# Kernel tuning notes

Hardware: AMD Instinct MI355X
Metric: run time of the kernel (lower is better)

The kernel has to match this reference:

```python
import math
import jax, jax.numpy as jnp
import numpy as np

S, K, Q, N, D, H = 512, 512, 64, 262144, 256, 8
DH = D // H
EPS = 1e-5


def layer_norm(x, g, b):
    mu = jnp.mean(x, axis=-1, keepdims=True)
    var = jnp.mean((x - mu) ** 2, axis=-1, keepdims=True)
    return (x - mu) / jnp.sqrt(var + EPS) * g + b


def setup_inputs() -> dict:
    key = jax.random.key(0)
    ks = jax.random.split(key, 12)
    s = 1.0 / math.sqrt(D)
    x = jax.random.normal(ks[0], (N, D), dtype=jnp.float32)
    target_ids = jax.random.randint(ks[1], (S, K), 0, N)
    # unique query slots per sample (matches torch per-slot overwrite with distinct ids)
    perm = jax.vmap(lambda k: jax.random.permutation(k, K))(jax.random.split(ks[2], S))
    add_ids = perm[:, :Q]
    return {
        "x": x,
        "target_ids": target_ids,
        "add_ids": add_ids,
        "Wq": jax.random.uniform(ks[3], (D, D), jnp.float32, -s, s),
        "bq": jnp.zeros((D,), jnp.float32),
        "Wk": jax.random.uniform(ks[4], (D, D), jnp.float32, -s, s),
        "bk": jnp.zeros((D,), jnp.float32),
        "Wv": jax.random.uniform(ks[5], (D, D), jnp.float32, -s, s),
        "bv": jnp.zeros((D,), jnp.float32),
        "g1": jnp.ones((D,), jnp.float32),
        "b1": jnp.zeros((D,), jnp.float32),
        "Wl": jax.random.uniform(ks[6], (D, D), jnp.float32, -s, s),
        "bl": jnp.zeros((D,), jnp.float32),
        "g2": jnp.ones((D,), jnp.float32),
        "b2": jnp.zeros((D,), jnp.float32),
    }


def reference(x, target_ids, add_ids, Wq, bq, Wk, bk, Wv, bv, g1, b1, Wl, bl, g2, b2):
    # gather per-sample node subsets
    key_t = x[target_ids]                                   # [S, K, D]
    query = jnp.take_along_axis(key_t, add_ids[:, :, None], axis=1)  # [S, Q, D]
    # MAB projections
    Qp = (query @ Wq.T + bq).reshape(S, Q, H, DH)
    Kp = (key_t @ Wk.T + bk).reshape(S, K, H, DH)
    Vp = (key_t @ Wv.T + bv).reshape(S, K, H, DH)
    # attention with original scaling by sqrt(dim_V) (full D, not per-head)
    scores = jnp.einsum("sqhd,skhd->shqk", Qp, Kp) / math.sqrt(D)
    A = jax.nn.softmax(scores, axis=-1)
    out = Qp + jnp.einsum("shqk,skhd->sqhd", A, Vp)          # residual on Q_
    out = out.reshape(S, Q, D)
    out = layer_norm(out, g1, b1)
    out = out + jax.nn.relu(out @ Wl.T + bl)
    out = layer_norm(out, g2, b2)                            # [S, Q, D]
    # scatter back into per-sample slots, then residual with key
    x_fuse = jnp.zeros((S, K, D), out.dtype)
    x_fuse = x_fuse.at[jnp.arange(S)[:, None], add_ids].set(out)
    x_fuse = x_fuse + key_t
    return x_fuse.reshape(S * K, D)
```

## Files before the change

kernel.cpp:

```cpp
#include <hip/hip_runtime.h>

#define S_ 512
#define K_ 512
#define Q_ 64
#define D_ 256
#define H_ 8
#define SK_ (S_*K_)
#define SQ_ (S_*Q_)

typedef float f32x4 __attribute__((ext_vector_type(4)));
typedef short bf16x8 __attribute__((ext_vector_type(8)));
typedef short bf16x4 __attribute__((ext_vector_type(4)));

__device__ __forceinline__ short f2bf(float f) {
  unsigned u = __builtin_bit_cast(unsigned, f);
  u += 0x7fffu + ((u >> 16) & 1u);
  return (short)(u >> 16);
}
__device__ __forceinline__ float bf2f(short s) {
  unsigned u = ((unsigned)(unsigned short)s) << 16;
  return __builtin_bit_cast(float, u);
}

__device__ __forceinline__ void async_copy16(short* lds, const short* g) {
  __builtin_amdgcn_global_load_lds(
      (const __attribute__((address_space(1))) void*)g,
      (__attribute__((address_space(3))) void*)lds, 16, 0, 0);
}

__global__ void cvt_w_kernel(const float* Wq, const float* Wk, const float* Wv,
                             const float* Wl, short* out) {
  int i = blockIdx.x * 256 + threadIdx.x;
  const float* src = (i < 65536) ? Wq : (i < 131072) ? Wk : (i < 196608) ? Wv : Wl;
  out[i] = f2bf(src[i & 65535]);
}

__global__ void gather_kernel(const float* x, const int* tid, short* kb) {
  int g = blockIdx.x * 256 + threadIdx.x;
  int row = g >> 5, e = (g & 31) * 8;
  int src = tid[row];
  f32x4 v0 = *(const f32x4*)(x + (size_t)src * 256 + e);
  f32x4 v1 = *(const f32x4*)(x + (size_t)src * 256 + e + 4);
  bf16x8 o;
#pragma unroll
  for (int j = 0; j < 4; j++) { o[j] = f2bf(v0[j]); o[j + 4] = f2bf(v1[j]); }
  *(bf16x8*)(kb + (size_t)row * 256 + e) = o;
}

__global__ void expand_kernel(const short* kb, float* dout) {
  int g = blockIdx.x * 256 + threadIdx.x;
  bf16x8 v = *(const bf16x8*)(kb + (size_t)g * 8);
  f32x4 a, b;
#pragma unroll
  for (int j = 0; j < 4; j++) { a[j] = bf2f(v[j]); b[j] = bf2f(v[j + 4]); }
  *(f32x4*)(dout + (size_t)g * 8) = a;
  *(f32x4*)(dout + (size_t)g * 8 + 4) = b;
}

template<int INDEXED, int CT>
__global__ __launch_bounds__(256, 2) void gemm2_kernel(const short* A, const int* aid,
                                                       const short* Wb, const float* bias,
                                                       short* Cp) {
  __shared__ short As[128 * 256];
  int w = threadIdx.x >> 6, lane = threadIdx.x & 63;
  int quad = lane >> 4, l16 = lane & 15;
  int rbase0 = blockIdx.x * 128;
  int colbase = w * 64;

  bf16x8 b[4][8];
#pragma unroll
  for (int nt = 0; nt < 4; nt++)
#pragma unroll
    for (int kk = 0; kk < 8; kk++)
      b[nt][kk] = *(const bf16x8*)(Wb + (colbase + nt * 16 + l16) * 256 + kk * 32 + quad * 8);
  float bv[4];
#pragma unroll
  for (int nt = 0; nt < 4; nt++) bv[nt] = bias[colbase + nt * 16 + l16];

  int cc = lane & 31;
#pragma unroll
  for (int i = 0; i < 16; i++) {
    int chunkLinear = w * 1024 + i * 64 + lane;
    int row = chunkLinear >> 5;
    int c = cc ^ (row & 15);
    int m = rbase0 + row;
    int arow = INDEXED ? (((m >> 6) << 9) + aid[m]) : m;
    async_copy16(As + (size_t)(w * 1024 + i * 64) * 8,
                 A + (size_t)arow * 256 + c * 8);
  }
  __syncthreads();

  for (int mt = 0; mt < 8; mt++) {
    bf16x8 a[8];
#pragma unroll
    for (int kk = 0; kk < 8; kk++)
      a[kk] = *(const bf16x8*)(As + (mt * 16 + l16) * 256 + (((kk * 4 + quad) ^ l16) * 8));
    f32x4 acc[4];
#pragma unroll
    for (int nt = 0; nt < 4; nt++) acc[nt] = (f32x4){bv[nt], bv[nt], bv[nt], bv[nt]};
#pragma unroll
    for (int kk = 0; kk < 8; kk++)
#pragma unroll
      for (int nt = 0; nt < 4; nt++)
        acc[nt] = __builtin_amdgcn_mfma_f32_16x16x32_bf16(a[kk], b[nt][kk], acc[nt], 0, 0, 0);

    int rbase = rbase0 + mt * 16;
    if (CT == 0) {
#pragma unroll
      for (int nt = 0; nt < 4; nt++) {
        int col = colbase + nt * 16 + l16;
#pragma unroll
        for (int r = 0; r < 4; r++)
          Cp[(size_t)(rbase + quad * 4 + r) * 256 + col] = f2bf(acc[nt][r]);
      }
    } else if (CT == 1) {
      int s = rbase >> 9;
      int keyb = (rbase & 511) + quad * 4;
#pragma unroll
      for (int nt = 0; nt < 4; nt++) {
        int col = colbase + nt * 16 + l16;
        int h = col >> 5, dh = col & 31;
        bf16x4 pk;
#pragma unroll
        for (int r = 0; r < 4; r++) pk[r] = f2bf(acc[nt][r]);
        *(bf16x4*)(Cp + ((((size_t)s * 8 + h) * 32 + dh) << 9) + keyb) = pk;
      }
    } else {
      int s = rbase >> 9;
      int keyb = (rbase & 511) + quad * 4;
#pragma unroll
      for (int nt = 0; nt < 4; nt++) {
        int col = colbase + nt * 16 + l16;
        int h = col >> 5, dh = col & 31;
        size_t basek = ((size_t)(s * 8 + h) * 512 + keyb) * 32 + dh;
#pragma unroll
        for (int r = 0; r < 4; r++)
          Cp[basek + (size_t)r * 32] = f2bf(acc[nt][r]);
      }
    }
  }
}

__global__ __launch_bounds__(256, 2) void attn_kernel(const short* Qp, const short* Kt,
                                                      const short* Vt, float* aout) {
  __shared__ short ldsK[16384];
  __shared__ short ldsV[16384];
  int bid = blockIdx.x;
  int s = bid >> 3, h = bid & 7;
  int w = threadIdx.x >> 6;
  int lane = threadIdx.x & 63;
  int quad = lane >> 4, l16 = lane & 15;

  const char* kb = (const char*)(Kt + ((size_t)bid << 14));
  const char* vb = (const char*)(Vt + ((size_t)bid << 14));
  char* lk = (char*)ldsK;
  char* lv = (char*)ldsV;

#pragma unroll
  for (int i = 0; i < 8; i++) {
    int ab = w * 8192 + i * 1024;
    int a = ab + lane * 16;
    async_copy16((short*)(lk + ab), (const short*)(kb + a));
    async_copy16((short*)(lv + ab), (const short*)(vb + (a ^ (((a >> 10) & 7) << 4))));
  }

  bf16x8 aq = *(const bf16x8*)(Qp + ((size_t)(s * 64 + w * 16 + l16)) * 256 + h * 32 + quad * 8);
  __syncthreads();

  f32x4 zero = (f32x4){0.f, 0.f, 0.f, 0.f};
  f32x4 sc[32];
#pragma unroll
  for (int nt = 0; nt < 32; nt++) {
    bf16x8 bk = *(const bf16x8*)(lk + (nt * 16 + l16) * 64 + quad * 16);
    sc[nt] = __builtin_amdgcn_mfma_f32_16x16x32_bf16(aq, bk, zero, 0, 0, 0);
  }

  float lsum[4];
#pragma unroll
  for (int r = 0; r < 4; r++) {
    float t[16];
#pragma unroll
    for (int i = 0; i < 16; i++) t[i] = fmaxf(sc[i][r], sc[i + 16][r]);
#pragma unroll
    for (int st = 8; st; st >>= 1)
#pragma unroll
      for (int i = 0; i < st; i++) t[i] = fmaxf(t[i], t[i + st]);
    float m = t[0];
#pragma unroll
    for (int off = 1; off < 16; off <<= 1) m = fmaxf(m, __shfl_xor(m, off, 64));
#pragma unroll
    for (int nt = 0; nt < 32; nt++) sc[nt][r] = __expf((sc[nt][r] - m) * 0.0625f);
    float u[16];
#pragma unroll
    for (int i = 0; i < 16; i++) u[i] = sc[i][r] + sc[i + 16][r];
#pragma unroll
    for (int st = 8; st; st >>= 1)
#pragma unroll
      for (int i = 0; i < st; i++) u[i] += u[i + st];
    float l = u[0];
#pragma unroll
    for (int off = 1; off < 16; off <<= 1) l += __shfl_xor(l, off, 64);
    lsum[r] = l;
  }

  __syncthreads();

  f32x4 o[2] = {zero, zero};
#pragma unroll
  for (int half = 0; half < 2; half++) {
#pragma unroll
    for (int nt = 0; nt < 16; nt++) {
      int ntg = half * 16 + nt;
#pragma unroll
      for (int r = 0; r < 4; r++) {
        int q = quad * 4 + r;
        *(short*)(lk + w * 8192 + q * 512 + ((nt * 32 + l16 * 2) ^ ((q & 7) << 4))) =
            f2bf(sc[ntg][r]);
      }
    }
#pragma unroll
    for (int kk = 0; kk < 8; kk++) {
      bf16x8 ap = *(const bf16x8*)(lk + w * 8192 + l16 * 512 +
                                   ((kk * 64 + quad * 16) ^ ((l16 & 7) << 4)));
#pragma unroll
      for (int nt2 = 0; nt2 < 2; nt2++) {
        int dh = nt2 * 16 + l16;
        const bf16x8* vp = (const bf16x8*)(lv + dh * 1024 +
            ((half * 512 + kk * 64 + quad * 16) ^ ((dh & 7) << 4)));
        o[nt2] = __builtin_amdgcn_mfma_f32_16x16x32_bf16(ap, *vp, o[nt2], 0, 0, 0);
      }
    }
  }

#pragma unroll
  for (int nt2 = 0; nt2 < 2; nt2++)
#pragma unroll
    for (int r = 0; r < 4; r++) {
      int q = w * 16 + quad * 4 + r;
      int dh = nt2 * 16 + l16;
      size_t oq = ((size_t)(s * 64 + q)) * 256 + h * 32 + dh;
      aout[oq] = bf2f(Qp[oq]) + o[nt2][r] / lsum[r];
    }
}

__global__ void ln1_kernel(const float* ain, const float* g1, const float* b1, short* out) {
  int g = blockIdx.x * 256 + threadIdx.x;
  int row = g >> 6, lane = g & 63;
  f32x4 v = *(const f32x4*)(ain + (size_t)row * 256 + lane * 4);
  float s = v[0] + v[1] + v[2] + v[3];
  float s2 = v[0]*v[0] + v[1]*v[1] + v[2]*v[2] + v[3]*v[3];
#pragma unroll
  for (int off = 1; off < 64; off <<= 1) { s += __shfl_xor(s, off, 64); s2 += __shfl_xor(s2, off, 64); }
  float mu = s * (1.f / 256.f);
  float var = s2 * (1.f / 256.f) - mu * mu;
  float inv = rsqrtf(var + 1e-5f);
  f32x4 gv = *(const f32x4*)(g1 + lane * 4);
  f32x4 bv = *(const f32x4*)(b1 + lane * 4);
  bf16x4 ov;
#pragma unroll
  for (int j = 0; j < 4; j++) ov[j] = f2bf((v[j] - mu) * inv * gv[j] + bv[j]);
  *(bf16x4*)(out + (size_t)row * 256 + lane * 4) = ov;
}

__global__ void ln2_kernel(const short* ln1, const short* tmp, const float* g2, const float* b2,
                           const int* aid, float* dout) {
  int g = blockIdx.x * 256 + threadIdx.x;
  int row = g >> 6, lane = g & 63;
  bf16x4 a = *(const bf16x4*)(ln1 + (size_t)row * 256 + lane * 4);
  bf16x4 t = *(const bf16x4*)(tmp + (size_t)row * 256 + lane * 4);
  float v[4];
#pragma unroll
  for (int j = 0; j < 4; j++) v[j] = bf2f(a[j]) + fmaxf(bf2f(t[j]), 0.f);
  float s = v[0] + v[1] + v[2] + v[3];
  float s2 = v[0]*v[0] + v[1]*v[1] + v[2]*v[2] + v[3]*v[3];
#pragma unroll
  for (int off = 1; off < 64; off <<= 1) { s += __shfl_xor(s, off, 64); s2 += __shfl_xor(s2, off, 64); }
  float mu = s * (1.f / 256.f);
  float var = s2 * (1.f / 256.f) - mu * mu;
  float inv = rsqrtf(var + 1e-5f);
  f32x4 gv = *(const f32x4*)(g2 + lane * 4);
  f32x4 bv = *(const f32x4*)(b2 + lane * 4);
  int sIdx = row >> 6;
  int tgt = aid[row];
  float* op = dout + ((size_t)(sIdx * 512 + tgt)) * 256 + lane * 4;
  f32x4 cur = *(f32x4*)op;
#pragma unroll
  for (int j = 0; j < 4; j++) cur[j] += (v[j] - mu) * inv * gv[j] + bv[j];
  *(f32x4*)op = cur;
}

extern "C" void kernel_launch(void* const* d_in, const int* in_sizes, int n_in,
                              void* d_out, int out_size, void* d_ws, size_t ws_size,
                              hipStream_t stream) {
  const float* x   = (const float*)d_in[0];
  const int* tid   = (const int*)d_in[1];
  const int* aid   = (const int*)d_in[2];
  const float* Wq  = (const float*)d_in[3];
  const float* bq  = (const float*)d_in[4];
  const float* Wk  = (const float*)d_in[5];
  const float* bk  = (const float*)d_in[6];
  const float* Wv  = (const float*)d_in[7];
  const float* bv  = (const float*)d_in[8];
  const float* g1  = (const float*)d_in[9];
  const float* b1  = (const float*)d_in[10];
  const float* Wl  = (const float*)d_in[11];
  const float* bl  = (const float*)d_in[12];
  const float* g2  = (const float*)d_in[13];
  const float* b2  = (const float*)d_in[14];
  float* out = (float*)d_out;

  char* base = (char*)d_ws;
  short* Wqb = (short*)base;
  short* Wkb = Wqb + 65536;
  short* Wvb = Wkb + 65536;
  short* Wlb = Wvb + 65536;
  size_t off = 4ull * 65536 * 2;
  short* kb   = (short*)(base + off); off += (size_t)SK_ * 256 * 2;
  short* Qpb  = (short*)(base + off); off += (size_t)SQ_ * 256 * 2;
  short* Kpb  = (short*)(base + off); off += (size_t)SK_ * 256 * 2;
  short* ln1b = Qpb;
  short* tmpb = Kpb;
  short* Vtb  = (short*)d_out;
  float* aout = (float*)((char*)d_out + (size_t)SK_ * 256 * 2);
  (void)ws_size; (void)in_sizes; (void)n_in; (void)out_size;

  cvt_w_kernel<<<1024, 256, 0, stream>>>(Wq, Wk, Wv, Wl, Wqb);
  gather_kernel<<<SK_ / 8, 256, 0, stream>>>(x, tid, kb);
  gemm2_kernel<0, 2><<<SK_ / 128, 256, 0, stream>>>(kb, nullptr, Wkb, bk, Kpb);
  gemm2_kernel<0, 1><<<SK_ / 128, 256, 0, stream>>>(kb, nullptr, Wvb, bv, Vtb);
  gemm2_kernel<1, 0><<<SQ_ / 128, 256, 0, stream>>>(kb, aid, Wqb, bq, Qpb);
  attn_kernel<<<S_ * H_, 256, 0, stream>>>(Qpb, Kpb, Vtb, aout);
  ln1_kernel<<<SQ_ / 4, 256, 0, stream>>>(aout, g1, b1, ln1b);
  gemm2_kernel<0, 0><<<SQ_ / 128, 256, 0, stream>>>(ln1b, nullptr, Wlb, bl, tmpb);
  expand_kernel<<<SK_ / 8, 256, 0, stream>>>(kb, out);
  ln2_kernel<<<SQ_ / 4, 256, 0, stream>>>(ln1b, tmpb, g2, b2, aid, out);
}
```

Measured before the change: 805.1 us.

## Fuse node gather with K and V projections into one kernel

Replaces the separate gather kernel and two projection GEMM launches with one kernel. It gathers x rows, converts them to bf16 and writes them both to global kb and to a swizzled LDS tile, then runs the K and V projections back-to-back from that shared tile. This removes two re-reads of the gathered bf16 rows from global memory and two kernel launches. The cost is a gather phase that stalls the GEMM and some extra register pressure from loading weights twice per block.

```diff
diff --git a/kernel.cpp b/kernel.cpp
--- a/kernel.cpp
+++ b/kernel.cpp
@@ -35,18 +35,6 @@
   out[i] = f2bf(src[i & 65535]);
 }
 
-__global__ void gather_kernel(const float* x, const int* tid, short* kb) {
-  int g = blockIdx.x * 256 + threadIdx.x;
-  int row = g >> 5, e = (g & 31) * 8;
-  int src = tid[row];
-  f32x4 v0 = *(const f32x4*)(x + (size_t)src * 256 + e);
-  f32x4 v1 = *(const f32x4*)(x + (size_t)src * 256 + e + 4);
-  bf16x8 o;
-#pragma unroll
-  for (int j = 0; j < 4; j++) { o[j] = f2bf(v0[j]); o[j + 4] = f2bf(v1[j]); }
-  *(bf16x8*)(kb + (size_t)row * 256 + e) = o;
-}
-
 __global__ void expand_kernel(const short* kb, float* dout) {
   int g = blockIdx.x * 256 + threadIdx.x;
   bf16x8 v = *(const bf16x8*)(kb + (size_t)g * 8);
@@ -57,7 +45,89 @@
   *(f32x4*)(dout + (size_t)g * 8 + 4) = b;
 }
 
-template<int INDEXED, int CT>
+__global__ __launch_bounds__(256, 2) void gkv_kernel(const float* x, const int* tid,
+                                                     const short* Wkb, const float* bkb,
+                                                     const short* Wvb, const float* bvb,
+                                                     short* kb, short* Kt, short* Vt) {
+  __shared__ short As[128 * 256];
+  int t = threadIdx.x;
+  int w = t >> 6, lane = t & 63, quad = lane >> 4, l16 = lane & 15;
+  int rbase0 = blockIdx.x * 128;
+  int colbase = w * 64;
+
+#pragma unroll
+  for (int i = 0; i < 16; i++) {
+    int g = i * 256 + t;
+    int row = g >> 5, c = g & 31;
+    int m = rbase0 + row;
+    int src = tid[m];
+    const float* xp = x + (size_t)src * 256 + c * 8;
+    f32x4 v0 = *(const f32x4*)xp;
+    f32x4 v1 = *(const f32x4*)(xp + 4);
+    bf16x8 o;
+#pragma unroll
+    for (int j = 0; j < 4; j++) { o[j] = f2bf(v0[j]); o[j + 4] = f2bf(v1[j]); }
+    *(bf16x8*)(kb + (size_t)m * 256 + c * 8) = o;
+    *(bf16x8*)(As + row * 256 + (c ^ (row & 15)) * 8) = o;
+  }
+  __syncthreads();
+
+#pragma unroll 1
+  for (int p = 0; p < 2; p++) {
+    const short* Wb = p ? Wvb : Wkb;
+    const float* bias = p ? bvb : bkb;
+    bf16x8 b[4][8];
+#pragma unroll
+    for (int nt = 0; nt < 4; nt++)
+#pragma unroll
+      for (int kk = 0; kk < 8; kk++)
+        b[nt][kk] = *(const bf16x8*)(Wb + (colbase + nt * 16 + l16) * 256 + kk * 32 + quad * 8);
+    float bv4[4];
+#pragma unroll
+    for (int nt = 0; nt < 4; nt++) bv4[nt] = bias[colbase + nt * 16 + l16];
+
+    for (int mt = 0; mt < 8; mt++) {
+      bf16x8 a[8];
+#pragma unroll
+      for (int kk = 0; kk < 8; kk++)
+        a[kk] = *(const bf16x8*)(As + (mt * 16 + l16) * 256 + (((kk * 4 + quad) ^ l16) * 8));
+      f32x4 acc[4];
+#pragma unroll
+      for (int nt = 0; nt < 4; nt++) acc[nt] = (f32x4){bv4[nt], bv4[nt], bv4[nt], bv4[nt]};
+#pragma unroll
+      for (int kk = 0; kk < 8; kk++)
+#pragma unroll
+        for (int nt = 0; nt < 4; nt++)
+          acc[nt] = __builtin_amdgcn_mfma_f32_16x16x32_bf16(a[kk], b[nt][kk], acc[nt], 0, 0, 0);
+
+      int rbase = rbase0 + mt * 16;
+      int s = rbase >> 9;
+      int keyb = (rbase & 511) + quad * 4;
+      if (p == 0) {
+#pragma unroll
+        for (int nt = 0; nt < 4; nt++) {
+          int col = colbase + nt * 16 + l16;
+          int h = col >> 5, dh = col & 31;
+          size_t basek = ((size_t)(s * 8 + h) * 512 + keyb) * 32 + dh;
+#pragma unroll
+          for (int r = 0; r < 4; r++) Kt[basek + (size_t)r * 32] = f2bf(acc[nt][r]);
+        }
+      } else {
+#pragma unroll
+        for (int nt = 0; nt < 4; nt++) {
+          int col = colbase + nt * 16 + l16;
+          int h = col >> 5, dh = col & 31;
+          bf16x4 pk;
+#pragma unroll
+          for (int r = 0; r < 4; r++) pk[r] = f2bf(acc[nt][r]);
+          *(bf16x4*)(Vt + ((((size_t)s * 8 + h) * 32 + dh) << 9) + keyb) = pk;
+        }
+      }
+    }
+  }
+}
+
+template<int INDEXED>
 __global__ __launch_bounds__(256, 2) void gemm2_kernel(const short* A, const int* aid,
                                                        const short* Wb, const float* bias,
                                                        short* Cp) {
@@ -105,38 +175,12 @@
         acc[nt] = __builtin_amdgcn_mfma_f32_16x16x32_bf16(a[kk], b[nt][kk], acc[nt], 0, 0, 0);
 
     int rbase = rbase0 + mt * 16;
-    if (CT == 0) {
-#pragma unroll
-      for (int nt = 0; nt < 4; nt++) {
-        int col = colbase + nt * 16 + l16;
-#pragma unroll
-        for (int r = 0; r < 4; r++)
-          Cp[(size_t)(rbase + quad * 4 + r) * 256 + col] = f2bf(acc[nt][r]);
-      }
-    } else if (CT == 1) {
-      int s = rbase >> 9;
-      int keyb = (rbase & 511) + quad * 4;
-#pragma unroll
-      for (int nt = 0; nt < 4; nt++) {
-        int col = colbase + nt * 16 + l16;
-        int h = col >> 5, dh = col & 31;
-        bf16x4 pk;
-#pragma unroll
-        for (int r = 0; r < 4; r++) pk[r] = f2bf(acc[nt][r]);
-        *(bf16x4*)(Cp + ((((size_t)s * 8 + h) * 32 + dh) << 9) + keyb) = pk;
-      }
-    } else {
-      int s = rbase >> 9;
-      int keyb = (rbase & 511) + quad * 4;
-#pragma unroll
-      for (int nt = 0; nt < 4; nt++) {
-        int col = colbase + nt * 16 + l16;
-        int h = col >> 5, dh = col & 31;
-        size_t basek = ((size_t)(s * 8 + h) * 512 + keyb) * 32 + dh;
-#pragma unroll
-        for (int r = 0; r < 4; r++)
-          Cp[basek + (size_t)r * 32] = f2bf(acc[nt][r]);
-      }
+#pragma unroll
+    for (int nt = 0; nt < 4; nt++) {
+      int col = colbase + nt * 16 + l16;
+#pragma unroll
+      for (int r = 0; r < 4; r++)
+        Cp[(size_t)(rbase + quad * 4 + r) * 256 + col] = f2bf(acc[nt][r]);
     }
   }
 }
@@ -325,13 +369,11 @@
   (void)ws_size; (void)in_sizes; (void)n_in; (void)out_size;
 
   cvt_w_kernel<<<1024, 256, 0, stream>>>(Wq, Wk, Wv, Wl, Wqb);
-  gather_kernel<<<SK_ / 8, 256, 0, stream>>>(x, tid, kb);
-  gemm2_kernel<0, 2><<<SK_ / 128, 256, 0, stream>>>(kb, nullptr, Wkb, bk, Kpb);
-  gemm2_kernel<0, 1><<<SK_ / 128, 256, 0, stream>>>(kb, nullptr, Wvb, bv, Vtb);
-  gemm2_kernel<1, 0><<<SQ_ / 128, 256, 0, stream>>>(kb, aid, Wqb, bq, Qpb);
+  gkv_kernel<<<SK_ / 128, 256, 0, stream>>>(x, tid, Wkb, bk, Wvb, bv, kb, Kpb, Vtb);
+  gemm2_kernel<1><<<SQ_ / 128, 256, 0, stream>>>(kb, aid, Wqb, bq, Qpb);
   attn_kernel<<<S_ * H_, 256, 0, stream>>>(Qpb, Kpb, Vtb, aout);
   ln1_kernel<<<SQ_ / 4, 256, 0, stream>>>(aout, g1, b1, ln1b);
-  gemm2_kernel<0, 0><<<SQ_ / 128, 256, 0, stream>>>(ln1b, nullptr, Wlb, bl, tmpb);
+  gemm2_kernel<0><<<SQ_ / 128, 256, 0, stream>>>(ln1b, nullptr, Wlb, bl, tmpb);
   expand_kernel<<<SK_ / 8, 256, 0, stream>>>(kb, out);
   ln2_kernel<<<SQ_ / 4, 256, 0, stream>>>(ln1b, tmpb, g2, b2, aid, out);
 }
```

Result: faster. 784.3 us (-2.6%).
